# Performance work log

Hardware: AMD Instinct MI355X
Metric: run time of the kernel (lower is better)

Reference implementation:

```python
import jax, jax.numpy as jnp
import numpy as np

NUM_CODES = 4096
CODE_DIM = 256
COMMITMENT_COST = 0.25
DIVERSITY_WEIGHT = 0.1
B = 65536


def setup_inputs() -> dict:
    key = jax.random.key(0)
    kz, ke = jax.random.split(key)
    z = jax.random.normal(kz, (B, CODE_DIM), dtype=jnp.float32)
    embedding = jax.random.normal(ke, (NUM_CODES, CODE_DIM), dtype=jnp.float32)
    return {"z": z, "embedding": embedding}


def reference(z, embedding):
    # distances [B, K] = ||z||^2 + ||e||^2 - 2 z e^T
    distances = (
        jnp.sum(z * z, axis=1, keepdims=True)
        + jnp.sum(embedding * embedding, axis=1)
        - 2.0 * z @ embedding.T
    )
    indices = jnp.argmin(distances, axis=1)  # [B] int
    z_q = embedding[indices]                  # [B, D]

    sg = jax.lax.stop_gradient
    commitment_loss = jnp.mean((z - sg(z_q)) ** 2)
    embedding_loss = jnp.mean((sg(z) - z_q) ** 2)

    # diversity regularizer over soft assignments
    soft = jax.nn.softmax(-distances, axis=1)        # [B, K]
    avg_soft = jnp.mean(soft, axis=0)                # [K]
    entropy = -jnp.sum(avg_soft * jnp.log(avg_soft + 1e-10))
    max_entropy = jnp.log(jnp.float32(NUM_CODES))
    diversity_loss = max_entropy - entropy

    vq_loss = (
        commitment_loss * COMMITMENT_COST
        + embedding_loss
        + DIVERSITY_WEIGHT * diversity_loss
    )

    # straight-through estimator
    z_q_st = z + sg(z_q - z)

    # perplexity from hard assignments (bincount == one-hot mean)
    avg_probs = jnp.bincount(indices, length=NUM_CODES).astype(jnp.float32) / B
    perplexity = jnp.exp(-jnp.sum(avg_probs * jnp.log(avg_probs + 1e-10)))

    return (z_q_st, vq_loss, perplexity, indices, diversity_loss)
```

## Files before the change

kernel.cpp:

```cpp
#include <hip/hip_runtime.h>
#include <cstdint>
#include <cstddef>


#define NROWS     65536
#define NCODES    4096
#define DDIM      256
#define CAND_CAP  24
#define UMARGIN   1.0f
#define USKIP     8.5f

typedef _Float16 half8 __attribute__((ext_vector_type(8)));
typedef _Float16 half4 __attribute__((ext_vector_type(4)));
typedef float    f32x4 __attribute__((ext_vector_type(4)));

#define WS_BINCNT   0u
#define WS_ZERO_END 16384u
#define WS_CANDCNT  16384u
#define WS_SPART    278528u
#define WS_EF16     8667136u
#define WS_EE       10764288u
#define WS_ROWD     10780672u
#define WS_CANDIDX  11042816u
#define WS_TE       17334272u
#define WS_TP       17367040u
#define WS_END      17399808u

__device__ __forceinline__ void gload_lds16(const void* g, void* lds) {
    __builtin_amdgcn_global_load_lds(
        (const __attribute__((address_space(1))) unsigned int*)g,
        (__attribute__((address_space(3))) unsigned int*)lds, 16, 0, 0);
}

__global__ __launch_bounds__(256)
void prep_kernel(const float* __restrict__ src, _Float16* __restrict__ dst,
                 float* __restrict__ norms)
{
    const int tid = threadIdx.x;
    const int w = tid >> 6, l = tid & 63;
    const int row = blockIdx.x * 4 + w;
    const float4 v = *(const float4*)(src + (size_t)row * DDIM + l * 4);
    half4 h;
    h[0] = (_Float16)v.x; h[1] = (_Float16)v.y;
    h[2] = (_Float16)v.z; h[3] = (_Float16)v.w;
    *(half4*)(dst + (size_t)row * DDIM + l * 4) = h;
    double s = (double)v.x * v.x + (double)v.y * v.y
             + (double)v.z * v.z + (double)v.w * v.w;
#pragma unroll
    for (int off = 1; off < 64; off <<= 1) s += __shfl_xor(s, off, 64);
    if (l == 0) norms[row] = (float)s;
}

__global__ __launch_bounds__(256, 3)
void sweep_fused_kernel(const float* __restrict__ z, const _Float16* __restrict__ ef,
                        const float* __restrict__ ee, float* __restrict__ Spart,
                        int* __restrict__ cand_cnt, int* __restrict__ cand_idx)
{
    __shared__ _Float16 Bl[2][32 * 256];
    __shared__ float Sl[NCODES];

    const int tid = threadIdx.x;
    const int w = tid >> 6, l = tid & 63;
    const int lg = l >> 4, lc = l & 15;
    const int row0 = blockIdx.x * 128;

    half8 af[2][8];
#pragma unroll
    for (int fr = 0; fr < 2; ++fr)
#pragma unroll
    for (int ksl = 0; ksl < 8; ++ksl) {
        const float* zp = z + (size_t)(row0 + w * 32 + fr * 16 + lc) * DDIM + ksl * 32 + lg * 8;
        const float4 v0 = *(const float4*)zp;
        const float4 v1 = *(const float4*)(zp + 4);
        half8 h;
        h[0] = (_Float16)v0.x; h[1] = (_Float16)v0.y; h[2] = (_Float16)v0.z; h[3] = (_Float16)v0.w;
        h[4] = (_Float16)v1.x; h[5] = (_Float16)v1.y; h[6] = (_Float16)v1.z; h[7] = (_Float16)v1.w;
        af[fr][ksl] = h;
    }

    for (int i = tid; i < NCODES; i += 256) Sl[i] = 0.0f;

    int soff[4];
#pragma unroll
    for (int it = 0; it < 4; ++it) {
        const int it_g = w * 4 + it;
        const int ksl = it_g >> 1, cf = it_g & 1;
        soff[it] = (cf * 16 + lc) * 512 + ksl * 64 + lg * 16;
    }
    const char* efb = (const char*)ef;
    char* blb = (char*)&Bl[0][0];

    float pmx[8], pZ[8];
#pragma unroll
    for (int i = 0; i < 8; ++i) { pmx[i] = -1e30f; pZ[i] = 0.0f; }
    int bcnt[8];
#pragma unroll
    for (int i = 0; i < 8; ++i) bcnt[i] = 0;

    float eevc[2];
#pragma unroll
    for (int cf = 0; cf < 2; ++cf) eevc[cf] = ee[cf * 16 + lc];
#pragma unroll
    for (int it = 0; it < 4; ++it)
        gload_lds16(efb + soff[it], blb + (w * 4 + it) * 1024);
    __syncthreads();

    for (int s = 0; s < 256; ++s) {
        const int cur = s & 1;
        const int nt = s & 127;
        const int nnt = (s + 1) & 127;

        float eevn[2];
#pragma unroll
        for (int cf = 0; cf < 2; ++cf) eevn[cf] = ee[nnt * 32 + cf * 16 + lc];

        if (s < 255) {
            const char* src = efb + ((size_t)nnt << 14);
            char* dst = blb + (cur ^ 1) * 16384;
#pragma unroll
            for (int it = 0; it < 4; ++it)
                gload_lds16(src + soff[it], dst + (w * 4 + it) * 1024);
        }

        const float eh0 = -0.5f * eevc[0], eh1 = -0.5f * eevc[1];
        f32x4 acc[2][2];
#pragma unroll
        for (int fr = 0; fr < 2; ++fr) {
            acc[fr][0] = (f32x4){eh0, eh0, eh0, eh0};
            acc[fr][1] = (f32x4){eh1, eh1, eh1, eh1};
        }

        const char* bb = blb + cur * 16384 + (l << 4);
        __builtin_amdgcn_s_setprio(1);
#pragma unroll
        for (int ksl = 0; ksl < 8; ++ksl) {
            const half8 b0 = *(const half8*)(bb + (ksl * 2 + 0) * 1024);
            const half8 b1 = *(const half8*)(bb + (ksl * 2 + 1) * 1024);
#pragma unroll
            for (int fr = 0; fr < 2; ++fr) {
                acc[fr][0] = __builtin_amdgcn_mfma_f32_16x16x32_f16(af[fr][ksl], b0, acc[fr][0], 0, 0, 0);
                acc[fr][1] = __builtin_amdgcn_mfma_f32_16x16x32_f16(af[fr][ksl], b1, acc[fr][1], 0, 0, 0);
            }
        }
        __builtin_amdgcn_s_setprio(0);

        if (s < 128) {
#pragma unroll
            for (int fr = 0; fr < 2; ++fr)
#pragma unroll
            for (int reg = 0; reg < 4; ++reg) {
                const int ri = fr * 4 + reg;
                const float u0 = acc[fr][0][reg];
                const float u1 = acc[fr][1][reg];
                const float mloc = fmaxf(u0, u1);
                float m = pmx[ri];
                if (mloc > m - USKIP) {
                    if (mloc > m) { pZ[ri] *= __expf(2.0f * (m - mloc)); m = mloc; pmx[ri] = m; }
                    pZ[ri] += __expf(2.0f * (u0 - m)) + __expf(2.0f * (u1 - m));
                }
            }
        } else {
            float sp[2] = {0.f, 0.f};
#pragma unroll
            for (int fr = 0; fr < 2; ++fr)
#pragma unroll
            for (int reg = 0; reg < 4; ++reg) {
                const int ri = fr * 4 + reg;
                const float m = pmx[ri], iz = pZ[ri];
#pragma unroll
                for (int cf = 0; cf < 2; ++cf) {
                    const float u = acc[fr][cf][reg];
                    const bool hit = (u >= m - UMARGIN);
                    const unsigned long long mk = __ballot(hit);
                    if (mk) {
                        const unsigned grp = (unsigned)((mk >> (lg * 16)) & 0xFFFFull);
                        const int slot = bcnt[ri] + __popc(grp & ((1u << lc) - 1u));
                        if (hit && slot < CAND_CAP) {
                            const int rg_ = row0 + w * 32 + fr * 16 + lg * 4 + reg;
                            cand_idx[(size_t)rg_ * CAND_CAP + slot] = nt * 32 + cf * 16 + lc;
                        }
                        bcnt[ri] += __popc(grp);
                    }
                    if (u >= m - USKIP) sp[cf] += __expf(2.0f * (u - m)) * iz;
                }
            }
#pragma unroll
            for (int cf = 0; cf < 2; ++cf) {
                float v = sp[cf];
                v += __shfl_xor(v, 16, 64);
                v += __shfl_xor(v, 32, 64);
                if (l < 16) atomicAdd(&Sl[nt * 32 + cf * 16 + l], v);
            }
        }

        if (s == 127) {
#pragma unroll
            for (int ri = 0; ri < 8; ++ri) {
                float m = pmx[ri], Zv = pZ[ri];
#pragma unroll
                for (int off = 1; off < 16; off <<= 1) {
                    const float mo = __shfl_xor(m, off, 64);
                    const float Zo = __shfl_xor(Zv, off, 64);
                    const float mn = fmaxf(m, mo);
                    Zv = Zv * __expf(2.0f * (m - mn)) + Zo * __expf(2.0f * (mo - mn));
                    m = mn;
                }
                pmx[ri] = m;
                pZ[ri] = 1.0f / Zv;
            }
        }

        __syncthreads();
        eevc[0] = eevn[0]; eevc[1] = eevn[1];
    }

    if (lc == 0) {
#pragma unroll
        for (int fr = 0; fr < 2; ++fr)
#pragma unroll
        for (int reg = 0; reg < 4; ++reg)
            cand_cnt[row0 + w * 32 + fr * 16 + lg * 4 + reg] = bcnt[fr * 4 + reg];
    }

    for (int i = tid; i < NCODES; i += 256)
        Spart[(size_t)blockIdx.x * NCODES + i] = Sl[i];
}

__global__ __launch_bounds__(256)
void refine_kernel(const float* __restrict__ z, const float* __restrict__ emb,
                   const int* __restrict__ cand_cnt, const int* __restrict__ cand_idx,
                   float* __restrict__ out_zq, float* __restrict__ out_idx,
                   unsigned int* __restrict__ bincnt, float* __restrict__ rowD)
{
    const int tid = threadIdx.x;
    const int w = tid >> 6, l = tid & 63;
    const int row = blockIdx.x * 4 + w;
    const float4 zv = *(const float4*)(z + (size_t)row * DDIM + l * 4);
    const double z0 = zv.x, z1 = zv.y, z2 = zv.z, z3 = zv.w;
    const int craw = cand_cnt[row];
    const int cnt = craw < 1 ? 1 : (craw > CAND_CAP ? CAND_CAP : craw);
    double dmin = 1e300; int kmin = 0;
    for (int c = 0; c < cnt; ++c) {
        int k = (craw < 1) ? 0 : cand_idx[(size_t)row * CAND_CAP + c];
        k &= (NCODES - 1);
        const float4 ev = *(const float4*)(emb + (size_t)k * DDIM + l * 4);
        const double t0 = z0 - ev.x, t1 = z1 - ev.y, t2 = z2 - ev.z, t3 = z3 - ev.w;
        double s = t0 * t0 + t1 * t1 + t2 * t2 + t3 * t3;
#pragma unroll
        for (int off = 1; off < 64; off <<= 1) s += __shfl_xor(s, off, 64);
        if (s < dmin || (s == dmin && k < kmin)) { dmin = s; kmin = k; }
    }
    const float4 bv = *(const float4*)(emb + (size_t)kmin * DDIM + l * 4);
    *(float4*)(out_zq + (size_t)row * DDIM + l * 4) = bv;
    if (l == 0) {
        out_idx[row] = (float)kmin;
        atomicAdd(&bincnt[kmin], 1u);
        rowD[row] = (float)dmin;
    }
}

__global__ __launch_bounds__(256)
void reduce1_kernel(const float* __restrict__ Spart, const unsigned int* __restrict__ bincnt,
                    const float* __restrict__ rowD,
                    double* __restrict__ te, double* __restrict__ tp, double* __restrict__ tm)
{
    const int k = blockIdx.x * 256 + threadIdx.x;
    double s = 0.0;
#pragma unroll 8
    for (int wg = 0; wg < 512; ++wg) s += (double)Spart[(size_t)wg * NCODES + k];
    const double avg = s * (1.0 / 65536.0);
    te[k] = avg * log(avg + 1e-10);
    const double ap = (double)bincnt[k] * (1.0 / 65536.0);
    tp[k] = ap * log(ap + 1e-10);
    double dm = 0.0;
#pragma unroll
    for (int j = 0; j < 16; ++j) dm += (double)rowD[k * 16 + j];
    tm[k] = dm;
}

__global__ __launch_bounds__(256)
void reduce2_kernel(const double* __restrict__ te, const double* __restrict__ tp,
                    const double* __restrict__ tm, float* __restrict__ out)
{
    __shared__ double sa[256], sb[256], sc[256];
    const int tid = threadIdx.x;
    double a = 0.0, b = 0.0, c = 0.0;
    for (int i = tid; i < NCODES; i += 256) { a += te[i]; b += tp[i]; c += tm[i]; }
    sa[tid] = a; sb[tid] = b; sc[tid] = c;
    __syncthreads();
    for (int s = 128; s > 0; s >>= 1) {
        if (tid < s) { sa[tid] += sa[tid + s]; sb[tid] += sb[tid + s]; sc[tid] += sc[tid + s]; }
        __syncthreads();
    }
    if (tid == 0) {
        const double entropy    = -sa[0];
        const double diversity  = log(4096.0) - entropy;
        const double perplexity = exp(-sb[0]);
        const double mse        = sc[0] * (1.0 / 16777216.0);
        const double vq         = 1.25 * mse + 0.1 * diversity;
        out[16777216] = (float)vq;
        out[16777217] = (float)perplexity;
        out[16842754] = (float)diversity;
    }
}

extern "C" void kernel_launch(void* const* d_in, const int* in_sizes, int n_in,
                              void* d_out, int out_size, void* d_ws, size_t ws_size,
                              hipStream_t stream)
{
    const float* z   = (const float*)d_in[0];
    const float* emb = (const float*)d_in[1];
    float* out = (float*)d_out;
    char* ws = (char*)d_ws;
    if (ws_size < (size_t)WS_END) return;

    unsigned int* bincnt   = (unsigned int*)(ws + WS_BINCNT);
    int*          cand_cnt = (int*)(ws + WS_CANDCNT);
    float*        Spart    = (float*)(ws + WS_SPART);
    _Float16*     ef16     = (_Float16*)(ws + WS_EF16);
    float*        ee       = (float*)(ws + WS_EE);
    float*        rowD     = (float*)(ws + WS_ROWD);
    int*          cand_idx = (int*)(ws + WS_CANDIDX);
    double*       te       = (double*)(ws + WS_TE);
    double*       tp       = (double*)(ws + WS_TP);
    double*       tm       = (double*)(ws + WS_CANDIDX);

    hipMemsetAsync(d_ws, 0, WS_ZERO_END, stream);
    hipLaunchKernelGGL(prep_kernel, dim3(NCODES / 4), dim3(256), 0, stream, emb, ef16, ee);
    hipLaunchKernelGGL(sweep_fused_kernel, dim3(NROWS / 128), dim3(256), 0, stream,
                       z, ef16, ee, Spart, cand_cnt, cand_idx);
    hipLaunchKernelGGL(refine_kernel, dim3(NROWS / 4), dim3(256), 0, stream,
                       z, emb, cand_cnt, cand_idx, out, out + 16777218, bincnt, rowD);
    hipLaunchKernelGGL(reduce1_kernel, dim3(16), dim3(256), 0, stream, Spart, bincnt, rowD, te, tp, tm);
    hipLaunchKernelGGL(reduce2_kernel, dim3(1), dim3(256), 0, stream, te, tp, tm, out);
}
```

Baseline: 481.6 us.

## Retile sweep kernel to 2x2 wave grid over 64-code tiles

The sweep kernel now arranges its four waves as 2 row-halves by 2 code-halves. Each wave holds 64 rows of z fragments and processes 32 codes per step over 64-code LDS tiles, which halves the loop trip count and the barriers, and doubles reuse of each B-fragment load. Per-row softmax max and sum partials are merged across the two code-half waves through LDS, and candidates are stored per half with cap 10 each. Refine gains an always-evaluated code 0 fallback. The cost is higher register pressure (occupancy forced to 2 waves/EU) and a smaller per-half candidate cap.

```diff
diff --git a/kernel.cpp b/kernel.cpp
--- a/kernel.cpp
+++ b/kernel.cpp
@@ -6,7 +6,8 @@
 #define NROWS     65536
 #define NCODES    4096
 #define DDIM      256
-#define CAND_CAP  24
+#define CAP_H     10
+#define CAND_STRIDE 20
 #define UMARGIN   1.0f
 #define USKIP     8.5f
 
@@ -17,14 +18,14 @@
 #define WS_BINCNT   0u
 #define WS_ZERO_END 16384u
 #define WS_CANDCNT  16384u
-#define WS_SPART    278528u
-#define WS_EF16     8667136u
-#define WS_EE       10764288u
-#define WS_ROWD     10780672u
-#define WS_CANDIDX  11042816u
-#define WS_TE       17334272u
-#define WS_TP       17367040u
-#define WS_END      17399808u
+#define WS_SPART    540672u
+#define WS_EF16     8929280u
+#define WS_EE       11026432u
+#define WS_ROWD     11042816u
+#define WS_CANDIDX  11304960u
+#define WS_TE       16547840u
+#define WS_TP       16580608u
+#define WS_END      16613376u
 
 __device__ __forceinline__ void gload_lds16(const void* g, void* lds) {
     __builtin_amdgcn_global_load_lds(
@@ -51,25 +52,26 @@
     if (l == 0) norms[row] = (float)s;
 }
 
-__global__ __launch_bounds__(256, 3)
+__global__ __attribute__((amdgpu_flat_work_group_size(256, 256), amdgpu_waves_per_eu(2, 2)))
 void sweep_fused_kernel(const float* __restrict__ z, const _Float16* __restrict__ ef,
                         const float* __restrict__ ee, float* __restrict__ Spart,
                         int* __restrict__ cand_cnt, int* __restrict__ cand_idx)
 {
-    __shared__ _Float16 Bl[2][32 * 256];
+    __shared__ _Float16 Bl[2][64 * 256];
     __shared__ float Sl[NCODES];
 
     const int tid = threadIdx.x;
     const int w = tid >> 6, l = tid & 63;
+    const int wm = w & 1, wn = w >> 1;
     const int lg = l >> 4, lc = l & 15;
     const int row0 = blockIdx.x * 128;
 
-    half8 af[2][8];
-#pragma unroll
-    for (int fr = 0; fr < 2; ++fr)
+    half8 af[4][8];
+#pragma unroll
+    for (int fr = 0; fr < 4; ++fr)
 #pragma unroll
     for (int ksl = 0; ksl < 8; ++ksl) {
-        const float* zp = z + (size_t)(row0 + w * 32 + fr * 16 + lc) * DDIM + ksl * 32 + lg * 8;
+        const float* zp = z + (size_t)(row0 + wm * 64 + fr * 16 + lc) * DDIM + ksl * 32 + lg * 8;
         const float4 v0 = *(const float4*)zp;
         const float4 v1 = *(const float4*)(zp + 4);
         half8 h;
@@ -80,73 +82,93 @@
 
     for (int i = tid; i < NCODES; i += 256) Sl[i] = 0.0f;
 
-    int soff[4];
-#pragma unroll
-    for (int it = 0; it < 4; ++it) {
-        const int it_g = w * 4 + it;
-        const int ksl = it_g >> 1, cf = it_g & 1;
+    int soff[8];
+#pragma unroll
+    for (int it = 0; it < 8; ++it) {
+        const int it_g = w * 8 + it;
+        const int ksl = it_g >> 2, cf = it_g & 3;
         soff[it] = (cf * 16 + lc) * 512 + ksl * 64 + lg * 16;
     }
     const char* efb = (const char*)ef;
     char* blb = (char*)&Bl[0][0];
 
-    float pmx[8], pZ[8];
-#pragma unroll
-    for (int i = 0; i < 8; ++i) { pmx[i] = -1e30f; pZ[i] = 0.0f; }
-    int bcnt[8];
-#pragma unroll
-    for (int i = 0; i < 8; ++i) bcnt[i] = 0;
+    float pmx[16], pZ[16];
+#pragma unroll
+    for (int i = 0; i < 16; ++i) { pmx[i] = -1e30f; pZ[i] = 0.0f; }
+    int bcnt[16];
+#pragma unroll
+    for (int i = 0; i < 16; ++i) bcnt[i] = 0;
 
     float eevc[2];
 #pragma unroll
-    for (int cf = 0; cf < 2; ++cf) eevc[cf] = ee[cf * 16 + lc];
-#pragma unroll
-    for (int it = 0; it < 4; ++it)
-        gload_lds16(efb + soff[it], blb + (w * 4 + it) * 1024);
+    for (int cf = 0; cf < 2; ++cf) eevc[cf] = ee[(wn * 2 + cf) * 16 + lc];
+#pragma unroll
+    for (int it = 0; it < 8; ++it)
+        gload_lds16(efb + soff[it], blb + (w * 8 + it) * 1024);
     __syncthreads();
 
-    for (int s = 0; s < 256; ++s) {
+    for (int s = 0; s < 128; ++s) {
         const int cur = s & 1;
-        const int nt = s & 127;
-        const int nnt = (s + 1) & 127;
+        const int nt = s & 63;
+        const int nnt = (s + 1) & 63;
+
+        if (s == 64) {
+#pragma unroll
+            for (int fr = 0; fr < 4; ++fr)
+#pragma unroll
+            for (int reg = 0; reg < 4; ++reg) {
+                const int ri = fr * 4 + reg;
+                const int rb = wm * 64 + fr * 16 + lg * 4 + reg;
+                const float m2 = Sl[(wn ^ 1) * 128 + rb];
+                const float Z2 = Sl[256 + (wn ^ 1) * 128 + rb];
+                const float m1 = pmx[ri], Z1 = pZ[ri];
+                const float mn = fmaxf(m1, m2);
+                const float Zt = Z1 * __expf(2.0f * (m1 - mn)) + Z2 * __expf(2.0f * (m2 - mn));
+                pmx[ri] = mn;
+                pZ[ri] = 1.0f / Zt;
+            }
+            __syncthreads();
+            if (tid < 512) Sl[tid] = 0.0f;
+            __syncthreads();
+        }
 
         float eevn[2];
 #pragma unroll
-        for (int cf = 0; cf < 2; ++cf) eevn[cf] = ee[nnt * 32 + cf * 16 + lc];
-
-        if (s < 255) {
-            const char* src = efb + ((size_t)nnt << 14);
-            char* dst = blb + (cur ^ 1) * 16384;
-#pragma unroll
-            for (int it = 0; it < 4; ++it)
-                gload_lds16(src + soff[it], dst + (w * 4 + it) * 1024);
+        for (int cf = 0; cf < 2; ++cf) eevn[cf] = ee[nnt * 64 + (wn * 2 + cf) * 16 + lc];
+
+        if (s < 127) {
+            const char* src = efb + ((size_t)nnt << 15);
+            char* dst = blb + (cur ^ 1) * 32768;
+#pragma unroll
+            for (int it = 0; it < 8; ++it)
+                gload_lds16(src + soff[it], dst + (w * 8 + it) * 1024);
         }
 
         const float eh0 = -0.5f * eevc[0], eh1 = -0.5f * eevc[1];
-        f32x4 acc[2][2];
-#pragma unroll
-        for (int fr = 0; fr < 2; ++fr) {
+        f32x4 acc[4][2];
+#pragma unroll
+        for (int fr = 0; fr < 4; ++fr) {
             acc[fr][0] = (f32x4){eh0, eh0, eh0, eh0};
             acc[fr][1] = (f32x4){eh1, eh1, eh1, eh1};
         }
 
-        const char* bb = blb + cur * 16384 + (l << 4);
+        const char* bb = blb + cur * 32768 + (l << 4) + wn * 2048;
         __builtin_amdgcn_s_setprio(1);
 #pragma unroll
         for (int ksl = 0; ksl < 8; ++ksl) {
-            const half8 b0 = *(const half8*)(bb + (ksl * 2 + 0) * 1024);
-            const half8 b1 = *(const half8*)(bb + (ksl * 2 + 1) * 1024);
-#pragma unroll
-            for (int fr = 0; fr < 2; ++fr) {
+            const half8 b0 = *(const half8*)(bb + (ksl * 4 + 0) * 1024);
+            const half8 b1 = *(const half8*)(bb + (ksl * 4 + 1) * 1024);
+#pragma unroll
+            for (int fr = 0; fr < 4; ++fr) {
                 acc[fr][0] = __builtin_amdgcn_mfma_f32_16x16x32_f16(af[fr][ksl], b0, acc[fr][0], 0, 0, 0);
                 acc[fr][1] = __builtin_amdgcn_mfma_f32_16x16x32_f16(af[fr][ksl], b1, acc[fr][1], 0, 0, 0);
             }
         }
         __builtin_amdgcn_s_setprio(0);
 
-        if (s < 128) {
-#pragma unroll
-            for (int fr = 0; fr < 2; ++fr)
+        if (s < 64) {
+#pragma unroll
+            for (int fr = 0; fr < 4; ++fr)
 #pragma unroll
             for (int reg = 0; reg < 4; ++reg) {
                 const int ri = fr * 4 + reg;
@@ -162,7 +184,7 @@
         } else {
             float sp[2] = {0.f, 0.f};
 #pragma unroll
-            for (int fr = 0; fr < 2; ++fr)
+            for (int fr = 0; fr < 4; ++fr)
 #pragma unroll
             for (int reg = 0; reg < 4; ++reg) {
                 const int ri = fr * 4 + reg;
@@ -175,9 +197,10 @@
                     if (mk) {
                         const unsigned grp = (unsigned)((mk >> (lg * 16)) & 0xFFFFull);
                         const int slot = bcnt[ri] + __popc(grp & ((1u << lc) - 1u));
-                        if (hit && slot < CAND_CAP) {
-                            const int rg_ = row0 + w * 32 + fr * 16 + lg * 4 + reg;
-                            cand_idx[(size_t)rg_ * CAND_CAP + slot] = nt * 32 + cf * 16 + lc;
+                        if (hit && slot < CAP_H) {
+                            const int rg_ = row0 + wm * 64 + fr * 16 + lg * 4 + reg;
+                            cand_idx[(size_t)rg_ * CAND_STRIDE + wn * CAP_H + slot]
+                                = nt * 64 + (wn * 2 + cf) * 16 + lc;
                         }
                         bcnt[ri] += __popc(grp);
                     }
@@ -189,13 +212,13 @@
                 float v = sp[cf];
                 v += __shfl_xor(v, 16, 64);
                 v += __shfl_xor(v, 32, 64);
-                if (l < 16) atomicAdd(&Sl[nt * 32 + cf * 16 + l], v);
-            }
-        }
-
-        if (s == 127) {
-#pragma unroll
-            for (int ri = 0; ri < 8; ++ri) {
+                if (l < 16) atomicAdd(&Sl[nt * 64 + (wn * 2 + cf) * 16 + l], v);
+            }
+        }
+
+        if (s == 63) {
+#pragma unroll
+            for (int ri = 0; ri < 16; ++ri) {
                 float m = pmx[ri], Zv = pZ[ri];
 #pragma unroll
                 for (int off = 1; off < 16; off <<= 1) {
@@ -206,7 +229,17 @@
                     m = mn;
                 }
                 pmx[ri] = m;
-                pZ[ri] = 1.0f / Zv;
+                pZ[ri] = Zv;
+            }
+            if (lc == 0) {
+#pragma unroll
+                for (int fr = 0; fr < 4; ++fr)
+#pragma unroll
+                for (int reg = 0; reg < 4; ++reg) {
+                    const int rb = wm * 64 + fr * 16 + lg * 4 + reg;
+                    Sl[wn * 128 + rb]       = pmx[fr * 4 + reg];
+                    Sl[256 + wn * 128 + rb] = pZ[fr * 4 + reg];
+                }
             }
         }
 
@@ -216,10 +249,10 @@
 
     if (lc == 0) {
 #pragma unroll
-        for (int fr = 0; fr < 2; ++fr)
+        for (int fr = 0; fr < 4; ++fr)
 #pragma unroll
         for (int reg = 0; reg < 4; ++reg)
-            cand_cnt[row0 + w * 32 + fr * 16 + lg * 4 + reg] = bcnt[fr * 4 + reg];
+            cand_cnt[(row0 + wm * 64 + fr * 16 + lg * 4 + reg) * 2 + wn] = bcnt[fr * 4 + reg];
     }
 
     for (int i = tid; i < NCODES; i += 256)
@@ -237,17 +270,22 @@
     const int row = blockIdx.x * 4 + w;
     const float4 zv = *(const float4*)(z + (size_t)row * DDIM + l * 4);
     const double z0 = zv.x, z1 = zv.y, z2 = zv.z, z3 = zv.w;
-    const int craw = cand_cnt[row];
-    const int cnt = craw < 1 ? 1 : (craw > CAND_CAP ? CAND_CAP : craw);
+    int c0 = cand_cnt[row * 2 + 0];
+    int c1 = cand_cnt[row * 2 + 1];
+    c0 = c0 < 0 ? 0 : (c0 > CAP_H ? CAP_H : c0);
+    c1 = c1 < 0 ? 0 : (c1 > CAP_H ? CAP_H : c1);
     double dmin = 1e300; int kmin = 0;
-    for (int c = 0; c < cnt; ++c) {
-        int k = (craw < 1) ? 0 : cand_idx[(size_t)row * CAND_CAP + c];
-        k &= (NCODES - 1);
+    for (int c = -1; c < c0 + c1; ++c) {
+        int k = 0;
+        if (c >= 0) {
+            const int off = (c < c0) ? c : (CAP_H + (c - c0));
+            k = cand_idx[(size_t)row * CAND_STRIDE + off] & (NCODES - 1);
+        }
         const float4 ev = *(const float4*)(emb + (size_t)k * DDIM + l * 4);
         const double t0 = z0 - ev.x, t1 = z1 - ev.y, t2 = z2 - ev.z, t3 = z3 - ev.w;
         double s = t0 * t0 + t1 * t1 + t2 * t2 + t3 * t3;
 #pragma unroll
-        for (int off = 1; off < 64; off <<= 1) s += __shfl_xor(s, off, 64);
+        for (int off2 = 1; off2 < 64; off2 <<= 1) s += __shfl_xor(s, off2, 64);
         if (s < dmin || (s == dmin && k < kmin)) { dmin = s; kmin = k; }
     }
     const float4 bv = *(const float4*)(emb + (size_t)kmin * DDIM + l * 4);
```

After: 577.8 us. 1.2x slower.
